# Kernel tuning notes

Measured on AMD Instinct MI355X. Metric: run time of the kernel, lower is better.

## Reference

```python
import jax, jax.numpy as jnp
import numpy as np

T, B, I, H = 512, 32, 512, 512

def setup_inputs() -> dict:
    key = jax.random.key(0)
    k1, k2, k3 = jax.random.split(key, 3)
    x = jax.random.normal(k1, (T, B, I), dtype=jnp.float32)
    h0 = jnp.zeros((B, H), dtype=jnp.float32)
    W_ih = jax.random.normal(k2, (3 * H, I), dtype=jnp.float32) * (1.0 / np.sqrt(H))
    # diagonal recurrent weights, one vector per gate (r, z, n), uniform(-1, 1)
    w_hh = jax.random.uniform(k3, (3, H), dtype=jnp.float32, minval=-1.0, maxval=1.0)
    return {"x": x, "h0": h0, "W_ih": W_ih, "w_hh": w_hh}

def reference(x, h0, W_ih, w_hh):
    # Precompute input-side gate pre-activations for all timesteps: (T, B, 3H)
    gx = jnp.einsum('tbi,gi->tbg', x, W_ih)
    xr, xz, xn = jnp.split(gx, 3, axis=-1)  # each (T, B, H)
    w_r, w_z, w_n = w_hh[0], w_hh[1], w_hh[2]  # each (H,)

    def step(h, g):
        gr, gz, gn = g
        r = jax.nn.sigmoid(gr + w_r * h)
        z = jax.nn.sigmoid(gz + w_z * h)
        n = jnp.tanh(gn + r * (w_n * h))
        h_new = (1.0 - z) * n + z * h
        return h_new, h_new

    h_last, out = jax.lax.scan(step, h0, (xr, xz, xn))
    # out: (T, B, H) all hidden states; h_last: (1, B, H) final state (GRU convention)
    return out, h_last[None, :, :]
```

## Files before the change

### kernel.cpp

```cpp
#include <hip/hip_runtime.h>
#include <hip/hip_bf16.h>
#include <stdint.h>

#define T_DIM 512
#define B_DIM 32
#define K_DIM 512
#define H_DIM 512
#define N_DIM 1536
#define M_DIM 16384

typedef __bf16 bf16_t;
typedef bf16_t bf16x8 __attribute__((ext_vector_type(8)));
typedef float floatx4 __attribute__((ext_vector_type(4)));

#define LOG2E 1.442695041f
#define TWO_LOG2E 2.885390082f

__device__ __forceinline__ unsigned int f2bf_bits(float f) {
  uint32_t u = __builtin_bit_cast(uint32_t, f);
  u += 0x7FFFu + ((u >> 16) & 1u);
  return u >> 16;
}

__global__ void convert_both_kernel(const float* __restrict__ x,
                                    unsigned short* __restrict__ xb,
                                    const float* __restrict__ W,
                                    unsigned short* __restrict__ Wb) {
  int bid = blockIdx.x;
  int i;
  const float* in;
  unsigned short* out;
  if (bid < 4096) {
    in = x; out = xb;
    i = (bid * 256 + threadIdx.x) * 8;
  } else {
    i = ((bid - 4096) * 256 + threadIdx.x) * 8;
    int rw = i >> 9;
    int k = i & 511;
    int g = rw >> 9;
    int h = rw & (H_DIM - 1);
    in = W;
    out = Wb + ((h * 3 + g) << 9) + k - i;
  }
  const float4* p = (const float4*)(in + i);
  float4 f0 = p[0];
  float4 f1 = p[1];
  uint4 v;
  v.x = f2bf_bits(f0.x) | (f2bf_bits(f0.y) << 16);
  v.y = f2bf_bits(f0.z) | (f2bf_bits(f0.w) << 16);
  v.z = f2bf_bits(f1.x) | (f2bf_bits(f1.y) << 16);
  v.w = f2bf_bits(f1.z) | (f2bf_bits(f1.w) << 16);
  *(uint4*)(out + i) = v;
}

__global__ __launch_bounds__(256) void gemm_bf16_kernel(
    const unsigned short* __restrict__ A, const unsigned short* __restrict__ Bm,
    float* __restrict__ C) {
  __shared__ bf16_t smem[16384];
  const int tid = threadIdx.x;
  const int lane = tid & 63;
  const int w = tid >> 6;
  const int tileM = blockIdx.x * 128;
  const int tileN = blockIdx.y * 128;
  const int waveM = w & 1;
  const int waveN = w >> 1;
  const int lm = lane & 15;
  const int lg = lane >> 4;

  floatx4 acc[4][4] = {};

  for (int k0 = 0; k0 < K_DIM; k0 += 64) {
#pragma unroll
    for (int j = 0; j < 4; ++j) {
      int s = j * 256 + tid;
      int row = s >> 3;
      int cpos = s & 7;
      int kc = cpos ^ (row & 7);
      bf16_t* la = smem + (j * 256 + w * 64) * 8;
      const unsigned short* ga = A + (size_t)(tileM + row) * K_DIM + k0 + kc * 8;
      __builtin_amdgcn_global_load_lds(
          (const __attribute__((address_space(1))) unsigned int*)ga,
          (__attribute__((address_space(3))) unsigned int*)la, 16, 0, 0);
      bf16_t* lb = smem + 8192 + (j * 256 + w * 64) * 8;
      const unsigned short* gb = Bm + (size_t)(tileN + row) * K_DIM + k0 + kc * 8;
      __builtin_amdgcn_global_load_lds(
          (const __attribute__((address_space(1))) unsigned int*)gb,
          (__attribute__((address_space(3))) unsigned int*)lb, 16, 0, 0);
    }
    __syncthreads();

#pragma unroll
    for (int ks = 0; ks < 2; ++ks) {
      bf16x8 af[4], bfg[4];
#pragma unroll
      for (int i = 0; i < 4; ++i) {
        int row = waveM * 64 + i * 16 + lm;
        int c = ks * 4 + lg;
        af[i] = *(const bf16x8*)(smem + row * 64 + (c ^ (row & 7)) * 8);
      }
#pragma unroll
      for (int j = 0; j < 4; ++j) {
        int row = waveN * 64 + j * 16 + lm;
        int c = ks * 4 + lg;
        bfg[j] = *(const bf16x8*)(smem + 8192 + row * 64 + (c ^ (row & 7)) * 8);
      }
#pragma unroll
      for (int i = 0; i < 4; ++i)
#pragma unroll
        for (int j = 0; j < 4; ++j)
          acc[i][j] = __builtin_amdgcn_mfma_f32_16x16x32_bf16(af[i], bfg[j],
                                                              acc[i][j], 0, 0, 0);
    }
    __syncthreads();
  }

  const int row0 = tileM + waveM * 64 + (lane >> 4) * 4;
  const int col0 = tileN + waveN * 64 + lm;
#pragma unroll
  for (int j = 0; j < 4; ++j) {
    const int col = col0 + j * 16;
    const float scl = (col % 3 == 2) ? TWO_LOG2E : -LOG2E;
#pragma unroll
    for (int i = 0; i < 4; ++i)
#pragma unroll
      for (int r = 0; r < 4; ++r)
        C[(size_t)(row0 + i * 16 + r) * N_DIM + col] = scl * acc[i][j][r];
  }
}

__global__ __launch_bounds__(64) void indgru_scan_kernel(
    const float* __restrict__ gx, const float* __restrict__ h0,
    const float* __restrict__ w_hh, float* __restrict__ out,
    float* __restrict__ hlast) {
  const int idx = blockIdx.x * 64 + threadIdx.x;
  const int b = idx >> 9;
  const int h = idx & (H_DIM - 1);
  const float wr = -LOG2E * w_hh[h];
  const float wz = -LOG2E * w_hh[H_DIM + h];
  const float wn = TWO_LOG2E * w_hh[2 * H_DIM + h];
  float hv = h0[idx];

  const float* base = gx + ((size_t)b * H_DIM + h) * 3;
  float* outp = out + (size_t)b * H_DIM + h;

  constexpr int D = 16;
  float pr[D], pz[D], pn[D];
#pragma unroll
  for (int t = 0; t < D; ++t) {
    const float* p = base + (size_t)t * (B_DIM * N_DIM);
    pr[t] = p[0];
    pz[t] = p[1];
    pn[t] = p[2];
  }

  for (int t0 = 0; t0 < T_DIM - D; t0 += D) {
#pragma unroll
    for (int s = 0; s < D; ++s) {
      const int t = t0 + s;
      float gr = pr[s], gz = pz[s], gn = pn[s];
      const float* p = base + (size_t)(t + D) * (B_DIM * N_DIM);
      pr[s] = p[0];
      pz[s] = p[1];
      pn[s] = p[2];
      asm volatile("" ::: "memory");
      float ar = fmaf(wr, hv, gr);
      float az = fmaf(wz, hv, gz);
      float t1 = wn * hv;
      float er = __builtin_amdgcn_exp2f(ar);
      float ez = __builtin_amdgcn_exp2f(az);
      float r = __builtin_amdgcn_rcpf(1.0f + er);
      float z = __builtin_amdgcn_rcpf(1.0f + ez);
      float en = __builtin_amdgcn_exp2f(fmaf(r, t1, gn));
      float u = __builtin_amdgcn_rcpf(1.0f + en);
      float n = fmaf(-2.0f, u, 1.0f);
      float zh = z * hv;
      float omz = 1.0f - z;
      hv = fmaf(n, omz, zh);
      outp[(size_t)t * (B_DIM * H_DIM)] = hv;
    }
  }
#pragma unroll
  for (int s = 0; s < D; ++s) {
    const int t = T_DIM - D + s;
    float ar = fmaf(wr, hv, pr[s]);
    float az = fmaf(wz, hv, pz[s]);
    float t1 = wn * hv;
    float er = __builtin_amdgcn_exp2f(ar);
    float ez = __builtin_amdgcn_exp2f(az);
    float r = __builtin_amdgcn_rcpf(1.0f + er);
    float z = __builtin_amdgcn_rcpf(1.0f + ez);
    float en = __builtin_amdgcn_exp2f(fmaf(r, t1, pn[s]));
    float u = __builtin_amdgcn_rcpf(1.0f + en);
    float n = fmaf(-2.0f, u, 1.0f);
    float zh = z * hv;
    float omz = 1.0f - z;
    hv = fmaf(n, omz, zh);
    outp[(size_t)t * (B_DIM * H_DIM)] = hv;
  }
  hlast[idx] = hv;
}

extern "C" void kernel_launch(void* const* d_in, const int* in_sizes, int n_in,
                              void* d_out, int out_size, void* d_ws, size_t ws_size,
                              hipStream_t stream) {
  const float* x    = (const float*)d_in[0];
  const float* h0   = (const float*)d_in[1];
  const float* W_ih = (const float*)d_in[2];
  const float* w_hh = (const float*)d_in[3];

  float* out = (float*)d_out;
  float* hlast = out + (size_t)T_DIM * B_DIM * H_DIM;

  char* ws = (char*)d_ws;
  unsigned short* xb = (unsigned short*)ws;
  unsigned short* Wb = (unsigned short*)(ws + 16777216);
  float* gx = (float*)(ws + 16777216 + 1572864);

  convert_both_kernel<<<4480, 256, 0, stream>>>(x, xb, W_ih, Wb);

  dim3 grid(M_DIM / 128, N_DIM / 128);
  gemm_bf16_kernel<<<grid, 256, 0, stream>>>(xb, Wb, gx);

  indgru_scan_kernel<<<256, 64, 0, stream>>>(gx, h0, w_hh, out, hlast);
}
```

Baseline: 163.1 us.

## Store gate pre-activations as fp16 with paired-hidden layout and staged epilogue

The GEMM output gx is now stored in fp16 instead of fp32, which halves the intermediate's write and read traffic. The column layout is interleaved so each pair of hidden units holds six contiguous gate values, and the scan kernel fetches all three gates with a single 8-byte load. The GEMM epilogue stages results through LDS so global stores are coalesced 8-byte writes. The cost is fp16 precision and range on the scaled pre-activations, plus extra bit-unpacking work in the scan.

```diff
diff --git a/kernel.cpp b/kernel.cpp
--- a/kernel.cpp
+++ b/kernel.cpp
@@ -27,22 +27,26 @@
                                     const float* __restrict__ W,
                                     unsigned short* __restrict__ Wb) {
   int bid = blockIdx.x;
+  const float* src;
+  unsigned short* dst;
   int i;
-  const float* in;
-  unsigned short* out;
   if (bid < 4096) {
-    in = x; out = xb;
     i = (bid * 256 + threadIdx.x) * 8;
+    src = x + i;
+    dst = xb + i;
   } else {
     i = ((bid - 4096) * 256 + threadIdx.x) * 8;
-    int rw = i >> 9;
+    int n = i >> 9;
     int k = i & 511;
-    int g = rw >> 9;
-    int h = rw & (H_DIM - 1);
-    in = W;
-    out = Wb + ((h * 3 + g) << 9) + k - i;
-  }
-  const float4* p = (const float4*)(in + i);
+    int p6 = n / 6;
+    int sub = n - p6 * 6;
+    int hodd = (sub >= 3) ? 1 : 0;
+    int g = sub - hodd * 3;
+    int h = p6 * 2 + hodd;
+    src = W + ((g << 9) + h) * 512 + k;
+    dst = Wb + i;
+  }
+  const float4* p = (const float4*)src;
   float4 f0 = p[0];
   float4 f1 = p[1];
   uint4 v;
@@ -50,12 +54,12 @@
   v.y = f2bf_bits(f0.z) | (f2bf_bits(f0.w) << 16);
   v.z = f2bf_bits(f1.x) | (f2bf_bits(f1.y) << 16);
   v.w = f2bf_bits(f1.z) | (f2bf_bits(f1.w) << 16);
-  *(uint4*)(out + i) = v;
+  *(uint4*)dst = v;
 }
 
 __global__ __launch_bounds__(256) void gemm_bf16_kernel(
     const unsigned short* __restrict__ A, const unsigned short* __restrict__ Bm,
-    float* __restrict__ C) {
+    _Float16* __restrict__ C) {
   __shared__ bf16_t smem[16384];
   const int tid = threadIdx.x;
   const int lane = tid & 63;
@@ -114,22 +118,34 @@
     __syncthreads();
   }
 
-  const int row0 = tileM + waveM * 64 + (lane >> 4) * 4;
-  const int col0 = tileN + waveN * 64 + lm;
+  _Float16* ep = (_Float16*)smem + w * 4096;
 #pragma unroll
   for (int j = 0; j < 4; ++j) {
-    const int col = col0 + j * 16;
-    const float scl = (col % 3 == 2) ? TWO_LOG2E : -LOG2E;
+    const int cl = lm + j * 16;
+    const int sub = (tileN + waveN * 64 + cl) % 6;
+    const float scl = (sub == 2 || sub == 5) ? TWO_LOG2E : -LOG2E;
 #pragma unroll
     for (int i = 0; i < 4; ++i)
 #pragma unroll
-      for (int r = 0; r < 4; ++r)
-        C[(size_t)(row0 + i * 16 + r) * N_DIM + col] = scl * acc[i][j][r];
+      for (int r = 0; r < 4; ++r) {
+        int rl = (lane >> 4) * 4 + r + 16 * i;
+        ep[rl * 64 + cl] = (_Float16)(scl * acc[i][j][r]);
+      }
+  }
+  const int q = lm;
+  const int rgrp = lane >> 4;
+  const size_t crow0 = (size_t)(tileM + waveM * 64);
+  const int ccol = tileN + waveN * 64 + q * 4;
+#pragma unroll
+  for (int k = 0; k < 16; ++k) {
+    int rl = rgrp + 4 * k;
+    uint2 v = *(const uint2*)(ep + rl * 64 + q * 4);
+    *(uint2*)(C + (crow0 + rl) * N_DIM + ccol) = v;
   }
 }
 
 __global__ __launch_bounds__(64) void indgru_scan_kernel(
-    const float* __restrict__ gx, const float* __restrict__ h0,
+    const _Float16* __restrict__ gx, const float* __restrict__ h0,
     const float* __restrict__ w_hh, float* __restrict__ out,
     float* __restrict__ hlast) {
   const int idx = blockIdx.x * 64 + threadIdx.x;
@@ -138,31 +154,34 @@
   const float wr = -LOG2E * w_hh[h];
   const float wz = -LOG2E * w_hh[H_DIM + h];
   const float wn = TWO_LOG2E * w_hh[2 * H_DIM + h];
+  const int sh = (h & 1) << 4;
   float hv = h0[idx];
 
-  const float* base = gx + ((size_t)b * H_DIM + h) * 3;
+  const char* base = (const char*)(gx + (size_t)b * N_DIM + (h >> 1) * 6) + ((h & 1) << 2);
   float* outp = out + (size_t)b * H_DIM + h;
 
   constexpr int D = 16;
-  float pr[D], pz[D], pn[D];
-#pragma unroll
-  for (int t = 0; t < D; ++t) {
-    const float* p = base + (size_t)t * (B_DIM * N_DIM);
-    pr[t] = p[0];
-    pz[t] = p[1];
-    pn[t] = p[2];
-  }
+  constexpr size_t TSTRIDE = (size_t)B_DIM * N_DIM * sizeof(_Float16);
+  uint2 pq[D];
+#pragma unroll
+  for (int t = 0; t < D; ++t)
+    pq[t] = *(const uint2*)(base + (size_t)t * TSTRIDE);
+
+  auto cvt16 = [](uint32_t bits) {
+    return (float)__builtin_bit_cast(_Float16, (unsigned short)bits);
+  };
 
   for (int t0 = 0; t0 < T_DIM - D; t0 += D) {
 #pragma unroll
     for (int s = 0; s < D; ++s) {
       const int t = t0 + s;
-      float gr = pr[s], gz = pz[s], gn = pn[s];
-      const float* p = base + (size_t)(t + D) * (B_DIM * N_DIM);
-      pr[s] = p[0];
-      pz[s] = p[1];
-      pn[s] = p[2];
+      uint2 q = pq[s];
+      pq[s] = *(const uint2*)(base + (size_t)(t + D) * TSTRIDE);
       asm volatile("" ::: "memory");
+      uint64_t v = (((uint64_t)q.y << 32) | q.x) >> sh;
+      float gr = cvt16((uint32_t)v);
+      float gz = cvt16((uint32_t)(v >> 16));
+      float gn = cvt16((uint32_t)(v >> 32));
       float ar = fmaf(wr, hv, gr);
       float az = fmaf(wz, hv, gz);
       float t1 = wn * hv;
@@ -182,14 +201,19 @@
 #pragma unroll
   for (int s = 0; s < D; ++s) {
     const int t = T_DIM - D + s;
-    float ar = fmaf(wr, hv, pr[s]);
-    float az = fmaf(wz, hv, pz[s]);
+    uint2 q = pq[s];
+    uint64_t v = (((uint64_t)q.y << 32) | q.x) >> sh;
+    float gr = cvt16((uint32_t)v);
+    float gz = cvt16((uint32_t)(v >> 16));
+    float gn = cvt16((uint32_t)(v >> 32));
+    float ar = fmaf(wr, hv, gr);
+    float az = fmaf(wz, hv, gz);
     float t1 = wn * hv;
     float er = __builtin_amdgcn_exp2f(ar);
     float ez = __builtin_amdgcn_exp2f(az);
     float r = __builtin_amdgcn_rcpf(1.0f + er);
     float z = __builtin_amdgcn_rcpf(1.0f + ez);
-    float en = __builtin_amdgcn_exp2f(fmaf(r, t1, pn[s]));
+    float en = __builtin_amdgcn_exp2f(fmaf(r, t1, gn));
     float u = __builtin_amdgcn_rcpf(1.0f + en);
     float n = fmaf(-2.0f, u, 1.0f);
     float zh = z * hv;
@@ -214,7 +238,7 @@
   char* ws = (char*)d_ws;
   unsigned short* xb = (unsigned short*)ws;
   unsigned short* Wb = (unsigned short*)(ws + 16777216);
-  float* gx = (float*)(ws + 16777216 + 1572864);
+  _Float16* gx = (_Float16*)(ws + 16777216 + 1572864);
 
   convert_both_kernel<<<4480, 256, 0, stream>>>(x, xb, W_ih, Wb);
 
```

Result: no change. 160.7 us (-1.5%).
